# Performance work log

Measured on AMD Instinct MI355X. Metric: run time of the kernel, lower is better.

The kernel has to match this reference:

```python
import jax, jax.numpy as jnp
import numpy as np

KX = jnp.array([[-1., 0., 1.], [-2., 0., 2.], [-1., 0., 1.]], dtype=jnp.float32).reshape(1, 1, 3, 3)
KY = jnp.array([[1., 2., 1.], [0., 0., 0.], [-1., -2., -1.]], dtype=jnp.float32).reshape(1, 1, 3, 3)

def _sobel(x, k):
    # x: [B,1,H,W], k: [1,1,3,3]; stride 1, padding 1 -> same spatial size
    return jax.lax.conv_general_dilated(
        x, k, window_strides=(1, 1), padding=((1, 1), (1, 1)),
        dimension_numbers=('NCHW', 'OIHW', 'NCHW'))

def setup_inputs() -> dict:
    key = jax.random.key(0)
    k1, k2 = jax.random.split(key)
    B, C, H, W = 32, 1, 512, 512
    output = jax.random.normal(k1, (B, C, H, W), dtype=jnp.float32)
    target = jax.random.normal(k2, (B, C, H, W), dtype=jnp.float32)
    return {"output": output, "target": target}

def reference(output, target):
    gx_t = _sobel(target, KX)
    gy_t = _sobel(target, KY)
    gx_o = _sobel(output, KX)
    gy_o = _sobel(output, KY)
    grad_loss = jnp.mean((gx_t - gx_o) ** 2) + jnp.mean((gy_t - gy_o) ** 2)
    return grad_loss
```

## Files before the change

### kernel.cpp

```cpp
#include <hip/hip_runtime.h>


#define BATCH 32
#define HH 512
#define WW 512
#define TR 16
#define TPB 256
#define NBLK (BATCH * (HH / TR))

typedef const __attribute__((address_space(1))) void* gas_ptr;
typedef __attribute__((address_space(3))) void* las_ptr;

__device__ __forceinline__ void async_copy16(const float* g, float* l) {
    __builtin_amdgcn_global_load_lds((gas_ptr)(const void*)g,
                                     (las_ptr)(void*)l, 16, 0, 0);
}

__global__ __launch_bounds__(TPB) void sobel_partial_kernel(
    const float* __restrict__ out_img,
    const float* __restrict__ tgt_img,
    float* __restrict__ partials)
{
    __shared__ float otile[TR + 2][WW];
    __shared__ float ttile[TR + 2][WW];
    __shared__ float wsum[TPB / 64];

    const int tid  = threadIdx.x;
    const int lane = tid & 63;
    const int wv   = tid >> 6;
    const int b    = (blockIdx.x & 7) * (NBLK / 8) + (blockIdx.x >> 3);
    const int img  = b >> 5;
    const int y0   = (b & 31) * TR;

    const size_t base = (size_t)img * HH * WW;

    const int top    = (y0 == 0);
    const int bot    = (y0 + TR == HH);
    const int srcRow0 = top ? 0 : y0 - 1;
    const int ldsRow0 = top ? 1 : 0;
    const int nchunk  = (TR + 2 - top - bot) * 2;
    const float* osrc = out_img + base + (size_t)srcRow0 * WW;
    const float* tsrc = tgt_img + base + (size_t)srcRow0 * WW;
    float* old = &otile[ldsRow0][0];
    float* tld = &ttile[ldsRow0][0];
    for (int c = wv; c < nchunk; c += 4) {
        const int off = c * 256 + lane * 4;
        async_copy16(osrc + off, old + off);
        async_copy16(tsrc + off, tld + off);
    }
    if (top) {
        if (tid < 128) *(float4*)&otile[0][tid * 4] = make_float4(0, 0, 0, 0);
        else           *(float4*)&ttile[0][(tid - 128) * 4] = make_float4(0, 0, 0, 0);
    }
    if (bot) {
        if (tid < 128) *(float4*)&otile[TR + 1][tid * 4] = make_float4(0, 0, 0, 0);
        else           *(float4*)&ttile[TR + 1][(tid - 128) * 4] = make_float4(0, 0, 0, 0);
    }
    __syncthreads();

    float s255 = 0.f, s256 = 0.f;
    if (lane < TR + 2) {
        s255 = ttile[lane][255] - otile[lane][255];
        s256 = ttile[lane][256] - otile[lane][256];
    }

    const int R0 = 4 * wv;
    float acc = 0.f;

#define ROWLOAD(dst, R)                                                     \
    {                                                                       \
        const float4 o4 = *(const float4*)&otile[(R)][cb];                  \
        const float4 t4 = *(const float4*)&ttile[(R)][cb];                  \
        dst = make_float4(t4.x - o4.x, t4.y - o4.y, t4.z - o4.z, t4.w - o4.w); \
    }
#define ROWPASS(hs, hd, d, R)                                               \
    {                                                                       \
        const float svL = __shfl(s255, (R), 64);                            \
        const float svR = __shfl(s256, (R), 64);                            \
        float dl = __shfl_up((d).w, 1, 64);                                 \
        float dr = __shfl_down((d).x, 1, 64);                               \
        if (lane == 0)  dl = h ? svL : 0.f;                                 \
        if (lane == 63) dr = h ? 0.f : svR;                                 \
        hs.x = fmaf(2.f, (d).x, dl + (d).y);      hd.x = (d).y - dl;        \
        hs.y = fmaf(2.f, (d).y, (d).x + (d).z);   hd.y = (d).z - (d).x;     \
        hs.z = fmaf(2.f, (d).z, (d).y + (d).w);   hd.z = (d).w - (d).y;     \
        hs.w = fmaf(2.f, (d).w, (d).z + dr);      hd.w = dr - (d).z;        \
    }
#define ACCUM(hsT, hdT, hsM, hdM, hsB, hdB)                                 \
    {                                                                       \
        float gx, gy;                                                       \
        gx = fmaf(2.f, hdM.x, hdT.x + hdB.x); gy = hsT.x - hsB.x;           \
        acc = fmaf(gx, gx, acc); acc = fmaf(gy, gy, acc);                   \
        gx = fmaf(2.f, hdM.y, hdT.y + hdB.y); gy = hsT.y - hsB.y;           \
        acc = fmaf(gx, gx, acc); acc = fmaf(gy, gy, acc);                   \
        gx = fmaf(2.f, hdM.z, hdT.z + hdB.z); gy = hsT.z - hsB.z;           \
        acc = fmaf(gx, gx, acc); acc = fmaf(gy, gy, acc);                   \
        gx = fmaf(2.f, hdM.w, hdT.w + hdB.w); gy = hsT.w - hsB.w;           \
        acc = fmaf(gx, gx, acc); acc = fmaf(gy, gy, acc);                   \
    }

    #pragma unroll
    for (int h = 0; h < 2; ++h) {
        const int cb = (h << 8) + lane * 4;
        float4 d0, d1, d2;
        float4 hs0, hd0, hs1, hd1, hs2, hd2;
        ROWLOAD(d0, R0 + 0); ROWPASS(hs0, hd0, d0, R0 + 0);
        ROWLOAD(d1, R0 + 1); ROWPASS(hs1, hd1, d1, R0 + 1);
        ROWLOAD(d2, R0 + 2); ROWPASS(hs2, hd2, d2, R0 + 2);
        ACCUM(hs0, hd0, hs1, hd1, hs2, hd2);
        ROWLOAD(d0, R0 + 3); ROWPASS(hs0, hd0, d0, R0 + 3);
        ACCUM(hs1, hd1, hs2, hd2, hs0, hd0);
        ROWLOAD(d1, R0 + 4); ROWPASS(hs1, hd1, d1, R0 + 4);
        ACCUM(hs2, hd2, hs0, hd0, hs1, hd1);
        ROWLOAD(d2, R0 + 5); ROWPASS(hs2, hd2, d2, R0 + 5);
        ACCUM(hs0, hd0, hs1, hd1, hs2, hd2);
    }
#undef ROWLOAD
#undef ROWPASS
#undef ACCUM

    #pragma unroll
    for (int off = 32; off > 0; off >>= 1)
        acc += __shfl_down(acc, off, 64);
    if (lane == 0) wsum[wv] = acc;
    __syncthreads();
    if (tid == 0)
        partials[b] = wsum[0] + wsum[1] + wsum[2] + wsum[3];
}

__global__ __launch_bounds__(TPB) void reduce_partials_kernel(
    const float* __restrict__ partials, float* __restrict__ out)
{
    const int tid = threadIdx.x;
    const float4 v = *(const float4*)(partials + tid * 4);
    float s = (v.x + v.y) + (v.z + v.w);
    #pragma unroll
    for (int off = 32; off > 0; off >>= 1)
        s += __shfl_down(s, off, 64);
    __shared__ float wsum[TPB / 64];
    if ((tid & 63) == 0) wsum[tid >> 6] = s;
    __syncthreads();
    if (tid == 0)
        out[0] = (wsum[0] + wsum[1] + wsum[2] + wsum[3])
               * (1.0f / ((float)BATCH * HH * WW));
}

extern "C" void kernel_launch(void* const* d_in, const int* in_sizes, int n_in,
                              void* d_out, int out_size, void* d_ws, size_t ws_size,
                              hipStream_t stream) {
    (void)in_sizes; (void)n_in; (void)ws_size; (void)out_size;
    const float* out_img = (const float*)d_in[0];
    const float* tgt_img = (const float*)d_in[1];
    float* partials = (float*)d_ws;
    float* res = (float*)d_out;

    sobel_partial_kernel<<<NBLK, TPB, 0, stream>>>(out_img, tgt_img, partials);
    reduce_partials_kernel<<<1, TPB, 0, stream>>>(partials, res);
}
```

Measured before the change: 19.72 us.

## Double-buffer strips in persistent blocks and fuse final reduction via atomic counter

Each block now processes four consecutive row strips of one image with 512 threads, prefetching the next strip into a second LDS buffer while computing the current one. The separate reduction kernel is replaced by a last-block-done pattern using an atomic counter that is reset with a memset before launch. This is meant to overlap global loads with compute and remove a kernel launch. In exchange the large LDS footprint limits the GPU to one block per CU, and a memset is added to the stream.

```diff
diff --git a/kernel.cpp b/kernel.cpp
--- a/kernel.cpp
+++ b/kernel.cpp
@@ -5,8 +5,10 @@
 #define HH 512
 #define WW 512
 #define TR 16
-#define TPB 256
-#define NBLK (BATCH * (HH / TR))
+#define NRW (TR + 2)
+#define TPB 512
+#define NBLK 256
+#define TPB_W (TPB / 64)
 
 typedef const __attribute__((address_space(1))) void* gas_ptr;
 typedef __attribute__((address_space(3))) void* las_ptr;
@@ -16,104 +18,114 @@
                                      (las_ptr)(void*)l, 16, 0, 0);
 }
 
-__global__ __launch_bounds__(TPB) void sobel_partial_kernel(
+__global__ __launch_bounds__(TPB) void sobel_loss_kernel(
     const float* __restrict__ out_img,
     const float* __restrict__ tgt_img,
-    float* __restrict__ partials)
+    float* __restrict__ partials,
+    unsigned* __restrict__ counter,
+    float* __restrict__ result)
 {
-    __shared__ float otile[TR + 2][WW];
-    __shared__ float ttile[TR + 2][WW];
-    __shared__ float wsum[TPB / 64];
+    __shared__ float tile[2][2][NRW * WW];
+    __shared__ float wsum[TPB_W];
+    __shared__ int   lastflag;
 
     const int tid  = threadIdx.x;
     const int lane = tid & 63;
     const int wv   = tid >> 6;
-    const int b    = (blockIdx.x & 7) * (NBLK / 8) + (blockIdx.x >> 3);
-    const int img  = b >> 5;
-    const int y0   = (b & 31) * TR;
-
+    const int b    = blockIdx.x;
+    const int img  = b >> 3;
+    const int strip0 = (b & 7) * 4;
     const size_t base = (size_t)img * HH * WW;
 
-    const int top    = (y0 == 0);
-    const int bot    = (y0 + TR == HH);
-    const int srcRow0 = top ? 0 : y0 - 1;
-    const int ldsRow0 = top ? 1 : 0;
-    const int nchunk  = (TR + 2 - top - bot) * 2;
-    const float* osrc = out_img + base + (size_t)srcRow0 * WW;
-    const float* tsrc = tgt_img + base + (size_t)srcRow0 * WW;
-    float* old = &otile[ldsRow0][0];
-    float* tld = &ttile[ldsRow0][0];
-    for (int c = wv; c < nchunk; c += 4) {
-        const int off = c * 256 + lane * 4;
-        async_copy16(osrc + off, old + off);
-        async_copy16(tsrc + off, tld + off);
-    }
-    if (top) {
-        if (tid < 128) *(float4*)&otile[0][tid * 4] = make_float4(0, 0, 0, 0);
-        else           *(float4*)&ttile[0][(tid - 128) * 4] = make_float4(0, 0, 0, 0);
-    }
-    if (bot) {
-        if (tid < 128) *(float4*)&otile[TR + 1][tid * 4] = make_float4(0, 0, 0, 0);
-        else           *(float4*)&ttile[TR + 1][(tid - 128) * 4] = make_float4(0, 0, 0, 0);
-    }
+    auto stage = [&](int dbuf, int strip) {
+        const int y0  = strip * TR;
+        const int top = (strip == 0);
+        const int bot = (strip == 31);
+        const int srcRow0 = top ? 0 : y0 - 1;
+        const int ldsRow0 = top ? 1 : 0;
+        const int nchunk  = (NRW - top - bot) * 2;
+        const float* osrc = out_img + base + (size_t)srcRow0 * WW;
+        const float* tsrc = tgt_img + base + (size_t)srcRow0 * WW;
+        float* od = &tile[dbuf][0][ldsRow0 * WW];
+        float* td = &tile[dbuf][1][ldsRow0 * WW];
+        for (int c = wv; c < nchunk; c += TPB_W) {
+            const int off = c * 256 + lane * 4;
+            async_copy16(osrc + off, od + off);
+            async_copy16(tsrc + off, td + off);
+        }
+        if (top) {
+            if (tid < 128)       *(float4*)&tile[dbuf][0][tid * 4] = make_float4(0,0,0,0);
+            else if (tid < 256)  *(float4*)&tile[dbuf][1][(tid-128) * 4] = make_float4(0,0,0,0);
+        }
+        if (bot) {
+            if (tid < 128)       *(float4*)&tile[dbuf][0][(NRW-1)*WW + tid * 4] = make_float4(0,0,0,0);
+            else if (tid < 256)  *(float4*)&tile[dbuf][1][(NRW-1)*WW + (tid-128) * 4] = make_float4(0,0,0,0);
+        }
+    };
+
+    stage(0, strip0);
     __syncthreads();
 
-    float s255 = 0.f, s256 = 0.f;
-    if (lane < TR + 2) {
-        s255 = ttile[lane][255] - otile[lane][255];
-        s256 = ttile[lane][256] - otile[lane][256];
+    float acc = 0.f;
+
+#define ROWLOAD(dst, R)                                                        \
+    {                                                                          \
+        const float4 o4 = *(const float4*)&ot[(R) * WW + cb];                  \
+        const float4 t4 = *(const float4*)&tt[(R) * WW + cb];                  \
+        dst = make_float4(t4.x - o4.x, t4.y - o4.y, t4.z - o4.z, t4.w - o4.w); \
+    }
+#define ROWPASS(hs, hd, d, R)                                                  \
+    {                                                                          \
+        const float svL = __shfl(s255, (R), 64);                               \
+        const float svR = __shfl(s256, (R), 64);                               \
+        float dl = __shfl_up((d).w, 1, 64);                                    \
+        float dr = __shfl_down((d).x, 1, 64);                                  \
+        if (lane == 0)  dl = h ? svL : 0.f;                                    \
+        if (lane == 63) dr = h ? 0.f : svR;                                    \
+        hs.x = fmaf(2.f, (d).x, dl + (d).y);      hd.x = (d).y - dl;           \
+        hs.y = fmaf(2.f, (d).y, (d).x + (d).z);   hd.y = (d).z - (d).x;        \
+        hs.z = fmaf(2.f, (d).z, (d).y + (d).w);   hd.z = (d).w - (d).y;        \
+        hs.w = fmaf(2.f, (d).w, (d).z + dr);      hd.w = dr - (d).z;           \
+    }
+#define ACCUM(hsT, hdT, hsM, hdM, hsB, hdB)                                    \
+    {                                                                          \
+        float gx, gy;                                                          \
+        gx = fmaf(2.f, hdM.x, hdT.x + hdB.x); gy = hsT.x - hsB.x;              \
+        acc = fmaf(gx, gx, acc); acc = fmaf(gy, gy, acc);                      \
+        gx = fmaf(2.f, hdM.y, hdT.y + hdB.y); gy = hsT.y - hsB.y;              \
+        acc = fmaf(gx, gx, acc); acc = fmaf(gy, gy, acc);                      \
+        gx = fmaf(2.f, hdM.z, hdT.z + hdB.z); gy = hsT.z - hsB.z;              \
+        acc = fmaf(gx, gx, acc); acc = fmaf(gy, gy, acc);                      \
+        gx = fmaf(2.f, hdM.w, hdT.w + hdB.w); gy = hsT.w - hsB.w;              \
+        acc = fmaf(gx, gx, acc); acc = fmaf(gy, gy, acc);                      \
     }
 
-    const int R0 = 4 * wv;
-    float acc = 0.f;
+    for (int t = 0; t < 4; ++t) {
+        if (t < 3) stage((t + 1) & 1, strip0 + t + 1);
 
-#define ROWLOAD(dst, R)                                                     \
-    {                                                                       \
-        const float4 o4 = *(const float4*)&otile[(R)][cb];                  \
-        const float4 t4 = *(const float4*)&ttile[(R)][cb];                  \
-        dst = make_float4(t4.x - o4.x, t4.y - o4.y, t4.z - o4.z, t4.w - o4.w); \
-    }
-#define ROWPASS(hs, hd, d, R)                                               \
-    {                                                                       \
-        const float svL = __shfl(s255, (R), 64);                            \
-        const float svR = __shfl(s256, (R), 64);                            \
-        float dl = __shfl_up((d).w, 1, 64);                                 \
-        float dr = __shfl_down((d).x, 1, 64);                               \
-        if (lane == 0)  dl = h ? svL : 0.f;                                 \
-        if (lane == 63) dr = h ? 0.f : svR;                                 \
-        hs.x = fmaf(2.f, (d).x, dl + (d).y);      hd.x = (d).y - dl;        \
-        hs.y = fmaf(2.f, (d).y, (d).x + (d).z);   hd.y = (d).z - (d).x;     \
-        hs.z = fmaf(2.f, (d).z, (d).y + (d).w);   hd.z = (d).w - (d).y;     \
-        hs.w = fmaf(2.f, (d).w, (d).z + dr);      hd.w = dr - (d).z;        \
-    }
-#define ACCUM(hsT, hdT, hsM, hdM, hsB, hdB)                                 \
-    {                                                                       \
-        float gx, gy;                                                       \
-        gx = fmaf(2.f, hdM.x, hdT.x + hdB.x); gy = hsT.x - hsB.x;           \
-        acc = fmaf(gx, gx, acc); acc = fmaf(gy, gy, acc);                   \
-        gx = fmaf(2.f, hdM.y, hdT.y + hdB.y); gy = hsT.y - hsB.y;           \
-        acc = fmaf(gx, gx, acc); acc = fmaf(gy, gy, acc);                   \
-        gx = fmaf(2.f, hdM.z, hdT.z + hdB.z); gy = hsT.z - hsB.z;           \
-        acc = fmaf(gx, gx, acc); acc = fmaf(gy, gy, acc);                   \
-        gx = fmaf(2.f, hdM.w, hdT.w + hdB.w); gy = hsT.w - hsB.w;           \
-        acc = fmaf(gx, gx, acc); acc = fmaf(gy, gy, acc);                   \
-    }
+        const float* ot = &tile[t & 1][0][0];
+        const float* tt = &tile[t & 1][1][0];
 
-    #pragma unroll
-    for (int h = 0; h < 2; ++h) {
-        const int cb = (h << 8) + lane * 4;
-        float4 d0, d1, d2;
-        float4 hs0, hd0, hs1, hd1, hs2, hd2;
-        ROWLOAD(d0, R0 + 0); ROWPASS(hs0, hd0, d0, R0 + 0);
-        ROWLOAD(d1, R0 + 1); ROWPASS(hs1, hd1, d1, R0 + 1);
-        ROWLOAD(d2, R0 + 2); ROWPASS(hs2, hd2, d2, R0 + 2);
-        ACCUM(hs0, hd0, hs1, hd1, hs2, hd2);
-        ROWLOAD(d0, R0 + 3); ROWPASS(hs0, hd0, d0, R0 + 3);
-        ACCUM(hs1, hd1, hs2, hd2, hs0, hd0);
-        ROWLOAD(d1, R0 + 4); ROWPASS(hs1, hd1, d1, R0 + 4);
-        ACCUM(hs2, hd2, hs0, hd0, hs1, hd1);
-        ROWLOAD(d2, R0 + 5); ROWPASS(hs2, hd2, d2, R0 + 5);
-        ACCUM(hs0, hd0, hs1, hd1, hs2, hd2);
+        float s255 = 0.f, s256 = 0.f;
+        if (lane < NRW) {
+            s255 = tt[lane * WW + 255] - ot[lane * WW + 255];
+            s256 = tt[lane * WW + 256] - ot[lane * WW + 256];
+        }
+
+        const int R0 = 2 * wv;
+        #pragma unroll
+        for (int h = 0; h < 2; ++h) {
+            const int cb = (h << 8) + lane * 4;
+            float4 d0, d1, d2;
+            float4 hs0, hd0, hs1, hd1, hs2, hd2;
+            ROWLOAD(d0, R0 + 0); ROWPASS(hs0, hd0, d0, R0 + 0);
+            ROWLOAD(d1, R0 + 1); ROWPASS(hs1, hd1, d1, R0 + 1);
+            ROWLOAD(d2, R0 + 2); ROWPASS(hs2, hd2, d2, R0 + 2);
+            ACCUM(hs0, hd0, hs1, hd1, hs2, hd2);
+            ROWLOAD(d0, R0 + 3); ROWPASS(hs0, hd0, d0, R0 + 3);
+            ACCUM(hs1, hd1, hs2, hd2, hs0, hd0);
+        }
+        __syncthreads();
     }
 #undef ROWLOAD
 #undef ROWPASS
@@ -124,25 +136,36 @@
         acc += __shfl_down(acc, off, 64);
     if (lane == 0) wsum[wv] = acc;
     __syncthreads();
-    if (tid == 0)
-        partials[b] = wsum[0] + wsum[1] + wsum[2] + wsum[3];
-}
+    if (tid == 0) {
+        float s = 0.f;
+        #pragma unroll
+        for (int k = 0; k < TPB_W; ++k) s += wsum[k];
+        __hip_atomic_store(&partials[b], s, __ATOMIC_RELEASE,
+                           __HIP_MEMORY_SCOPE_AGENT);
+        const unsigned old = __hip_atomic_fetch_add(counter, 1u,
+                                                    __ATOMIC_ACQ_REL,
+                                                    __HIP_MEMORY_SCOPE_AGENT);
+        lastflag = (old == NBLK - 1);
+    }
+    __syncthreads();
 
-__global__ __launch_bounds__(TPB) void reduce_partials_kernel(
-    const float* __restrict__ partials, float* __restrict__ out)
-{
-    const int tid = threadIdx.x;
-    const float4 v = *(const float4*)(partials + tid * 4);
-    float s = (v.x + v.y) + (v.z + v.w);
-    #pragma unroll
-    for (int off = 32; off > 0; off >>= 1)
-        s += __shfl_down(s, off, 64);
-    __shared__ float wsum[TPB / 64];
-    if ((tid & 63) == 0) wsum[tid >> 6] = s;
-    __syncthreads();
-    if (tid == 0)
-        out[0] = (wsum[0] + wsum[1] + wsum[2] + wsum[3])
-               * (1.0f / ((float)BATCH * HH * WW));
+    if (lastflag) {
+        float s = (tid < NBLK)
+            ? __hip_atomic_load(&partials[tid], __ATOMIC_RELAXED,
+                                __HIP_MEMORY_SCOPE_AGENT)
+            : 0.f;
+        #pragma unroll
+        for (int off = 32; off > 0; off >>= 1)
+            s += __shfl_down(s, off, 64);
+        if (lane == 0) wsum[wv] = s;
+        __syncthreads();
+        if (tid == 0) {
+            float v = 0.f;
+            #pragma unroll
+            for (int k = 0; k < TPB_W; ++k) v += wsum[k];
+            result[0] = v * (1.0f / ((float)BATCH * HH * WW));
+        }
+    }
 }
 
 extern "C" void kernel_launch(void* const* d_in, const int* in_sizes, int n_in,
@@ -151,9 +174,11 @@
     (void)in_sizes; (void)n_in; (void)ws_size; (void)out_size;
     const float* out_img = (const float*)d_in[0];
     const float* tgt_img = (const float*)d_in[1];
-    float* partials = (float*)d_ws;
+    float* partials   = (float*)d_ws;
+    unsigned* counter = (unsigned*)((char*)d_ws + NBLK * sizeof(float));
     float* res = (float*)d_out;
 
-    sobel_partial_kernel<<<NBLK, TPB, 0, stream>>>(out_img, tgt_img, partials);
-    reduce_partials_kernel<<<1, TPB, 0, stream>>>(partials, res);
+    hipMemsetAsync(counter, 0, sizeof(unsigned), stream);
+    sobel_loss_kernel<<<NBLK, TPB, 0, stream>>>(out_img, tgt_img,
+                                                partials, counter, res);
 }
```

New measurement: 31.20 us. 58.2% more time.
